# Performance work log

Measured on AMD Instinct MI355X. Metric: run time of the kernel, lower is better.

## Reference

```python
import jax, jax.numpy as jnp
import numpy as np
import math

H, W = 32, 32
HEAD = 8
ZONE = 2
D_MODEL = 512
BT, N, C = 8, H * W, D_MODEL
T = 4


def setup_inputs() -> dict:
    key = jax.random.key(0)
    ks = jax.random.split(key, 9)
    s = 1.0 / math.sqrt(D_MODEL)
    inp = {
        "x": jax.random.normal(ks[0], (BT, N, C), dtype=jnp.float32),
        "t": T,
        "Wq": jax.random.normal(ks[1], (C, C), dtype=jnp.float32) * s,
        "bq": jnp.zeros((C,), dtype=jnp.float32),
        "Wk": jax.random.normal(ks[2], (C, C), dtype=jnp.float32) * s,
        "bk": jnp.zeros((C,), dtype=jnp.float32),
        "Wv": jax.random.normal(ks[3], (C, C), dtype=jnp.float32) * s,
        "bv": jnp.zeros((C,), dtype=jnp.float32),
        "Wo": jax.random.normal(ks[4], (C, C), dtype=jnp.float32) * s,
        "bo": jnp.zeros((C,), dtype=jnp.float32),
    }
    return inp


def _to_windows(y, b, t, c_h):
    # [bt, n, c] -> [b, zone^2, head, t*(h/z)*(w/z), c_h]
    y = y.reshape(b, t, ZONE, H // ZONE, ZONE, W // ZONE, HEAD, c_h)
    y = jnp.transpose(y, (0, 2, 4, 6, 1, 3, 5, 7))
    return y.reshape(b, ZONE * ZONE, HEAD, -1, c_h)


def reference(x, t, Wq, bq, Wk, bk, Wv, bv, Wo, bo):
    bt, n, c = x.shape
    b = bt // t
    c_h = c // HEAD
    q = x @ Wq.T + bq
    k = x @ Wk.T + bk
    v = x @ Wv.T + bv
    q = _to_windows(q, b, t, c_h)  # [b, z^2, head, L, c_h]
    k = _to_windows(k, b, t, c_h)
    v = _to_windows(v, b, t, c_h)
    scores = jnp.einsum('bzhlc,bzhmc->bzhlm', q, k) / math.sqrt(c_h)
    p = jax.nn.softmax(scores, axis=-1)
    att = jnp.einsum('bzhlm,bzhmc->bzhlc', p, v)  # [b, z^2, head, L, c_h]
    att = att.reshape(b, ZONE, ZONE, HEAD, t, H // ZONE, W // ZONE, c_h)
    att = jnp.transpose(att, (0, 4, 1, 5, 2, 6, 3, 7)).reshape(bt, n, c)
    return att @ Wo.T + bo
```

## Files before the change

### kernel.cpp

```cpp
#include <hip/hip_runtime.h>
#include <math.h>
#include <stdint.h>


typedef unsigned short u16;
typedef unsigned int u32;
typedef __attribute__((ext_vector_type(8))) short bf16x8;
typedef __attribute__((ext_vector_type(4))) float f32x4;
typedef __attribute__((ext_vector_type(16))) float f32x16;

__device__ __forceinline__ u16 f2b(float f) {
  u32 u = __float_as_uint(f);
  return (u16)((u + 0x7FFFu + ((u >> 16) & 1u)) >> 16);
}

__device__ __forceinline__ void gld_lds16(const void* g, void* l) {
  auto gp = (__attribute__((address_space(1))) u32*)(uintptr_t)g;
  auto lp = (__attribute__((address_space(3))) u32*)(u32)(uintptr_t)l;
  __builtin_amdgcn_global_load_lds(gp, lp, 16, 0, 0);
}

__global__ __launch_bounds__(256)
void prep_cvt(const float* __restrict__ x, const float* __restrict__ wq,
              const float* __restrict__ wk, const float* __restrict__ wv,
              const float* __restrict__ wo, u16* __restrict__ xb,
              u16* __restrict__ wqb, u16* __restrict__ wkb,
              u16* __restrict__ wvb, u16* __restrict__ wob)
{
  int i = blockIdx.x * 256 + threadIdx.x;
  const float* src; u16* dst; int off;
  if (i < 1048576) { src = x; dst = xb; off = i; }
  else {
    int j = i - 1048576; int w = j >> 16; off = j & 65535;
    src = (w == 0) ? wq : (w == 1) ? wk : (w == 2) ? wv : wo;
    dst = (w == 0) ? wqb : (w == 1) ? wkb : (w == 2) ? wvb : wob;
  }
  float4 v = ((const float4*)src)[off];
  ushort4 o;
  o.x = f2b(v.x); o.y = f2b(v.y); o.z = f2b(v.z); o.w = f2b(v.w);
  ((ushort4*)dst)[off] = o;
}

__global__ __launch_bounds__(256, 2)
void gemm_qkv(const u16* __restrict__ A, const u16* __restrict__ Bq,
              const u16* __restrict__ Bk, const u16* __restrict__ Bv,
              const float* __restrict__ bq, const float* __restrict__ bk,
              const float* __restrict__ bv, u16* __restrict__ qw,
              u16* __restrict__ kw, u16* __restrict__ vt)
{
  __shared__ u16 As[2][8192];
  __shared__ u16 Ws[3][2][4096];
  const int tid = threadIdx.x;
  const int lane = tid & 63;
  const int wbase = (tid & 192) * 8;
  const int m0 = blockIdx.y * 128, n0 = blockIdx.x * 64;
  const int wm = ((tid >> 7) & 1) * 64;
  const int wn = ((tid >> 6) & 1) * 32;
  const int arow = tid >> 3, aslot = tid & 7;

  f32x4 accq[4][2], acck[4][2], accv[4][2];
#pragma unroll
  for (int i = 0; i < 4; ++i)
#pragma unroll
    for (int j = 0; j < 2; ++j) {
#pragma unroll
      for (int r = 0; r < 4; ++r) { accq[i][j][r] = 0.f; acck[i][j][r] = 0.f; accv[i][j][r] = 0.f; }
    }

  auto stage = [&](int t, int buf) {
#pragma unroll
    for (int q = 0; q < 4; ++q) {
      int row = q * 32 + arow;
      int sl = aslot ^ (row & 7);
      gld_lds16(A + (size_t)(m0 + row) * 512 + t * 64 + sl * 8,
                &As[buf][q * 2048 + wbase]);
    }
    const u16* bp[3] = {Bq, Bk, Bv};
#pragma unroll
    for (int w = 0; w < 3; ++w)
#pragma unroll
      for (int q = 0; q < 2; ++q) {
        int row = q * 32 + arow;
        int sl = aslot ^ (row & 7);
        gld_lds16(bp[w] + (size_t)(n0 + row) * 512 + t * 64 + sl * 8,
                  &Ws[w][buf][q * 2048 + wbase]);
      }
  };

  stage(0, 0);
  __syncthreads();
  int cur = 0;
#pragma unroll 1
  for (int t = 0; t < 8; ++t) {
    if (t < 7) stage(t + 1, cur ^ 1);
    const u16* la = As[cur];
    bf16x8 af[4][2];
#pragma unroll
    for (int mf = 0; mf < 4; ++mf)
#pragma unroll
      for (int ks = 0; ks < 2; ++ks) {
        int row = wm + mf * 16 + (lane & 15);
        int s = ks * 4 + (lane >> 4);
        af[mf][ks] = *(const bf16x8*)(la + row * 64 + ((s ^ (row & 7)) << 3));
      }
    __builtin_amdgcn_s_setprio(1);
#pragma unroll
    for (int ks = 0; ks < 2; ++ks)
#pragma unroll
      for (int nf = 0; nf < 2; ++nf) {
        int row = wn + nf * 16 + (lane & 15);
        int s = ks * 4 + (lane >> 4);
        int boff = row * 64 + ((s ^ (row & 7)) << 3);
        bf16x8 bq8 = *(const bf16x8*)(Ws[0][cur] + boff);
        bf16x8 bk8 = *(const bf16x8*)(Ws[1][cur] + boff);
        bf16x8 bv8 = *(const bf16x8*)(Ws[2][cur] + boff);
#pragma unroll
        for (int mf = 0; mf < 4; ++mf) {
          accq[mf][nf] = __builtin_amdgcn_mfma_f32_16x16x32_bf16(af[mf][ks], bq8, accq[mf][nf], 0, 0, 0);
          acck[mf][nf] = __builtin_amdgcn_mfma_f32_16x16x32_bf16(af[mf][ks], bk8, acck[mf][nf], 0, 0, 0);
          accv[mf][nf] = __builtin_amdgcn_mfma_f32_16x16x32_bf16(af[mf][ks], bv8, accv[mf][nf], 0, 0, 0);
        }
      }
    __builtin_amdgcn_s_setprio(0);
    __syncthreads();
    cur ^= 1;
  }

  int h[2], d[2]; float bqv[2], bkv[2], bvv[2];
#pragma unroll
  for (int nf = 0; nf < 2; ++nf) {
    int col = n0 + wn + nf * 16 + (lane & 15);
    h[nf] = col >> 6; d[nf] = col & 63;
    bqv[nf] = bq[col]; bkv[nf] = bk[col]; bvv[nf] = bv[col];
  }
#pragma unroll
  for (int mf = 0; mf < 4; ++mf) {
    int mb = m0 + wm + mf * 16 + ((lane >> 4) << 2);
    int b = mb >> 12, t = (mb >> 10) & 3, row32 = (mb >> 5) & 31, col32 = mb & 31;
    int zi = row32 >> 4, hirow = row32 & 15, zj = col32 >> 4, wj = col32 & 15;
    int gb = b * 32 + (zi * 2 + zj) * 8;
    int l0 = t * 256 + hirow * 16 + wj;
#pragma unroll
    for (int nf = 0; nf < 2; ++nf) {
      size_t qkbase = ((size_t)(gb + h[nf]) * 1024 + l0) * 64 + d[nf];
#pragma unroll
      for (int r = 0; r < 4; ++r) {
        qw[qkbase + (size_t)r * 64] = f2b(accq[mf][nf][r] + bqv[nf]);
        kw[qkbase + (size_t)r * 64] = f2b(acck[mf][nf][r] + bkv[nf]);
      }
      ushort4 pv;
      pv.x = f2b(accv[mf][nf][0] + bvv[nf]);
      pv.y = f2b(accv[mf][nf][1] + bvv[nf]);
      pv.z = f2b(accv[mf][nf][2] + bvv[nf]);
      pv.w = f2b(accv[mf][nf][3] + bvv[nf]);
      *(ushort4*)(vt + ((size_t)(gb + h[nf]) * 64 + d[nf]) * 1024 + l0) = pv;
    }
  }
}

__global__ __launch_bounds__(256)
void attn32(const u16* __restrict__ qw, const u16* __restrict__ kw,
            const u16* __restrict__ vt, u16* __restrict__ attb)
{
  __shared__ u16 Kl[3][4096];
  __shared__ u16 Vl[3][4096];

  const int tid = threadIdx.x, lane = tid & 63, wid = tid >> 6;
  const int hi = lane >> 5, ln = lane & 31;
  const int n = blockIdx.x;
  const int work = (n & 7) * 64 + (n >> 3);
  const int g = work >> 3, qt = work & 7;
  const int b = g >> 5, z = (g >> 3) & 3, h = g & 7, zi = z >> 1, zj = z & 1;
  const u16* qg = qw + (size_t)g * 65536;
  const u16* kg = kw + (size_t)g * 65536;
  const u16* vg = vt + (size_t)g * 65536;
  const int q0 = qt * 128 + wid * 32;
  const float SC2 = 0.125f * 1.44269504089f;
  const float SHIFT = -20.f;

  const int t8 = lane >> 3, s8 = lane & 7;

  auto stageKV = [&](int c, int buf) {
#pragma unroll
    for (int p = 0; p < 2; ++p) {
      int row = wid * 16 + p * 8 + t8;
      gld_lds16(kg + (size_t)(c * 64 + row) * 64 + ((s8 ^ (row & 7)) << 3),
                Kl[buf] + wid * 1024 + p * 512);
      gld_lds16(vg + (size_t)row * 1024 + c * 64 + ((s8 ^ (row & 7)) << 3),
                Vl[buf] + wid * 1024 + p * 512);
    }
  };

  bf16x8 qf[4];
#pragma unroll
  for (int ks = 0; ks < 4; ++ks)
    qf[ks] = *(const bf16x8*)(qg + (size_t)(q0 + ln) * 64 + ks * 16 + hi * 8);

  f32x16 o[2];
#pragma unroll
  for (int nf = 0; nf < 2; ++nf)
#pragma unroll
    for (int r = 0; r < 16; ++r) o[nf][r] = 0.f;
  float lrun = 0.f;

  stageKV(0, 0);
  stageKV(1, 1);
  asm volatile("s_waitcnt vmcnt(4)" ::: "memory");
  __builtin_amdgcn_s_barrier();
  __builtin_amdgcn_sched_barrier(0);

  int cur = 0, pre = 2;

#pragma unroll 1
  for (int c = 0; c < 16; ++c) {
    if (c < 14) stageKV(c + 2, pre);

    bf16x8 kk[2][4];
#pragma unroll
    for (int kb = 0; kb < 2; ++kb)
#pragma unroll
      for (int ks = 0; ks < 4; ++ks) {
        int row = kb * 32 + ln;
        int sl = (ks * 2 + hi) ^ (ln & 7);
        kk[kb][ks] = *(const bf16x8*)(Kl[cur] + row * 64 + sl * 8);
      }

    f32x16 st[2];
#pragma unroll
    for (int kb = 0; kb < 2; ++kb)
#pragma unroll
      for (int r = 0; r < 16; ++r) st[kb][r] = 0.f;
    __builtin_amdgcn_s_setprio(1);
#pragma unroll
    for (int ks = 0; ks < 4; ++ks) {
      st[0] = __builtin_amdgcn_mfma_f32_32x32x16_bf16(kk[0][ks], qf[ks], st[0], 0, 0, 0);
      st[1] = __builtin_amdgcn_mfma_f32_32x32x16_bf16(kk[1][ks], qf[ks], st[1], 0, 0, 0);
    }
    __builtin_amdgcn_s_setprio(0);

    float racc[4] = {0.f, 0.f, 0.f, 0.f};
#pragma unroll
    for (int kb = 0; kb < 2; ++kb)
#pragma unroll
      for (int r = 0; r < 16; ++r) {
        float p = exp2f(fmaf(st[kb][r], SC2, SHIFT));
        st[kb][r] = p;
        racc[r & 3] += p;
      }
    float rs = (racc[0] + racc[1]) + (racc[2] + racc[3]);
    rs += __shfl_xor(rs, 32);
    lrun += rs;

    u32 W[2][4][2];
#pragma unroll
    for (int kb = 0; kb < 2; ++kb)
#pragma unroll
      for (int j = 0; j < 4; ++j)
#pragma unroll
        for (int u = 0; u < 2; ++u) {
          u32 w;
          asm("v_cvt_pk_bf16_f32 %0, %1, %2"
              : "=v"(w) : "v"(st[kb][4 * j + 2 * u]), "v"(st[kb][4 * j + 2 * u + 1]));
          W[kb][j][u] = w;
        }
    __builtin_amdgcn_s_setprio(1);
#pragma unroll
    for (int ks = 0; ks < 4; ++ks) {
      const int kb = ks >> 1, sl2 = ks & 1;
      u32 a0 = W[kb][2 * sl2][0], b0 = W[kb][2 * sl2 + 1][0];
      u32 a1 = W[kb][2 * sl2][1], b1 = W[kb][2 * sl2 + 1][1];
      asm volatile("v_permlane32_swap_b32 %0, %1" : "+v"(a0), "+v"(b0));
      asm volatile("v_permlane32_swap_b32 %0, %1" : "+v"(a1), "+v"(b1));
      union { u32 u[4]; bf16x8 v; } pu;
      pu.u[0] = a0; pu.u[1] = a1; pu.u[2] = b0; pu.u[3] = b1;
#pragma unroll
      for (int nf = 0; nf < 2; ++nf) {
        int drow = nf * 32 + ln;
        int vsl = (ks * 2 + hi) ^ (ln & 7);
        bf16x8 vf = *(const bf16x8*)(Vl[cur] + drow * 64 + vsl * 8);
        o[nf] = __builtin_amdgcn_mfma_f32_32x32x16_bf16(pu.v, vf, o[nf], 0, 0, 0);
      }
    }
    __builtin_amdgcn_s_setprio(0);

    if (c < 15) {
      if (c < 14) { asm volatile("s_waitcnt vmcnt(4)" ::: "memory"); }
      else        { asm volatile("s_waitcnt vmcnt(0)" ::: "memory"); }
      __builtin_amdgcn_s_barrier();
      __builtin_amdgcn_sched_barrier(0);
    }
    cur = (cur == 2) ? 0 : cur + 1;
    pre = (pre == 2) ? 0 : pre + 1;
  }

  const int rowbase = b * 4096 + zi * 512 + zj * 16;
  const int colbase = h * 64;
#pragma unroll
  for (int r = 0; r < 16; ++r) {
    int qr = (r & 3) + 8 * (r >> 2) + 4 * hi;
    float lv = __shfl(lrun, qr);
    float iv = 1.f / lv;
    int l = q0 + qr;
    int row = rowbase + ((l >> 8) << 10) + (((l >> 4) & 15) << 5) + (l & 15);
    size_t off = (size_t)row * 512 + colbase + ln;
    attb[off] = f2b(o[0][r] * iv);
    attb[off + 32] = f2b(o[1][r] * iv);
  }
}

__global__ __launch_bounds__(256, 2)
void gemm_o(const u16* __restrict__ A, const u16* __restrict__ B,
            const float* __restrict__ bias, float* __restrict__ Cout)
{
  __shared__ u16 lds[2][12288];
  const int tid = threadIdx.x;
  const int lane = tid & 63;
  const int wbase = (tid & 192) * 8;
  const int m0 = blockIdx.y * 128, n0 = blockIdx.x * 64;
  const int wm = ((tid >> 7) & 1) * 64;
  const int wn = ((tid >> 6) & 1) * 32;
  const int arow = tid >> 3, aslot = tid & 7;

  f32x4 acc[4][2];
#pragma unroll
  for (int i = 0; i < 4; ++i)
#pragma unroll
    for (int j = 0; j < 2; ++j)
#pragma unroll
      for (int r = 0; r < 4; ++r) acc[i][j][r] = 0.f;

  auto stage = [&](int t, int buf) {
#pragma unroll
    for (int q = 0; q < 4; ++q) {
      int row = q * 32 + arow;
      int sl = aslot ^ (row & 7);
      gld_lds16(A + (size_t)(m0 + row) * 512 + t * 64 + sl * 8,
                &lds[buf][q * 2048 + wbase]);
    }
#pragma unroll
    for (int q = 0; q < 2; ++q) {
      int row = q * 32 + arow;
      int sl = aslot ^ (row & 7);
      gld_lds16(B + (size_t)(n0 + row) * 512 + t * 64 + sl * 8,
                &lds[buf][8192 + q * 2048 + wbase]);
    }
  };

  stage(0, 0);
  __syncthreads();
  int cur = 0;
#pragma unroll 1
  for (int t = 0; t < 8; ++t) {
    if (t < 7) stage(t + 1, cur ^ 1);
    const u16* la = lds[cur];
    const u16* lb = lds[cur] + 8192;
    bf16x8 af[4][2];
#pragma unroll
    for (int mf = 0; mf < 4; ++mf)
#pragma unroll
      for (int ks = 0; ks < 2; ++ks) {
        int row = wm + mf * 16 + (lane & 15);
        int s = ks * 4 + (lane >> 4);
        af[mf][ks] = *(const bf16x8*)(la + row * 64 + ((s ^ (row & 7)) << 3));
      }
    __builtin_amdgcn_s_setprio(1);
#pragma unroll
    for (int ks = 0; ks < 2; ++ks)
#pragma unroll
      for (int nf = 0; nf < 2; ++nf) {
        int row = wn + nf * 16 + (lane & 15);
        int s = ks * 4 + (lane >> 4);
        bf16x8 bfr = *(const bf16x8*)(lb + row * 64 + ((s ^ (row & 7)) << 3));
#pragma unroll
        for (int mf = 0; mf < 4; ++mf)
          acc[mf][nf] = __builtin_amdgcn_mfma_f32_16x16x32_bf16(af[mf][ks], bfr, acc[mf][nf], 0, 0, 0);
      }
    __builtin_amdgcn_s_setprio(0);
    __syncthreads();
    cur ^= 1;
  }

#pragma unroll
  for (int mf = 0; mf < 4; ++mf)
#pragma unroll
    for (int nf = 0; nf < 2; ++nf) {
      int row = m0 + wm + mf * 16 + ((lane >> 4) << 2);
      int col = n0 + wn + nf * 16 + (lane & 15);
      float bi = bias[col];
#pragma unroll
      for (int r = 0; r < 4; ++r)
        Cout[(size_t)(row + r) * 512 + col] = acc[mf][nf][r] + bi;
    }
}

extern "C" void kernel_launch(void* const* d_in, const int* in_sizes, int n_in,
                              void* d_out, int out_size, void* d_ws, size_t ws_size,
                              hipStream_t stream) {
  const float* x  = (const float*)d_in[0];
  const float* Wq = (const float*)d_in[2];
  const float* bq = (const float*)d_in[3];
  const float* Wk = (const float*)d_in[4];
  const float* bk = (const float*)d_in[5];
  const float* Wv = (const float*)d_in[6];
  const float* bv = (const float*)d_in[7];
  const float* Wo = (const float*)d_in[8];
  const float* bo = (const float*)d_in[9];

  u16* xb   = (u16*)d_ws;
  u16* wqb  = xb + 4194304;
  u16* wkb  = wqb + 262144;
  u16* wvb  = wkb + 262144;
  u16* wob  = wvb + 262144;
  u16* qwb  = wob + 262144;
  u16* kwb  = qwb + 4194304;
  u16* vtb  = kwb + 4194304;
  u16* attb = vtb + 4194304;

  prep_cvt<<<5120, 256, 0, stream>>>(x, Wq, Wk, Wv, Wo, xb, wqb, wkb, wvb, wob);
  gemm_qkv<<<dim3(8, 64), 256, 0, stream>>>(xb, wqb, wkb, wvb, bq, bk, bv, qwb, kwb, vtb);
  attn32<<<512, 256, 0, stream>>>(qwb, kwb, vtb, attb);
  gemm_o<<<dim3(8, 64), 256, 0, stream>>>(attb, wob, bo, (float*)d_out);
}
```

Before: 86.56 us.

## Process KV chunks in pairs with double-buffered LDS and two blocks per CU

Restructures the attention loop so each iteration handles two 64-key chunks. Both QK^T products are issued before the two softmax/PV stages, which gives more independent MFMA work to interleave. The LDS buffering changes from a 3-deep ring to a double buffer of chunk pairs, which halves the number of barriers per key. It also adds a launch bound of 2 blocks per CU, so register use is capped and the kernel may spill. The waits now drain all loads (vmcnt(0)) before each barrier, which could expose load latency.

```diff
diff --git a/kernel.cpp b/kernel.cpp
--- a/kernel.cpp
+++ b/kernel.cpp
@@ -158,12 +158,12 @@
   }
 }
 
-__global__ __launch_bounds__(256)
+__global__ __launch_bounds__(256, 2)
 void attn32(const u16* __restrict__ qw, const u16* __restrict__ kw,
             const u16* __restrict__ vt, u16* __restrict__ attb)
 {
-  __shared__ u16 Kl[3][4096];
-  __shared__ u16 Vl[3][4096];
+  __shared__ u16 Kl[2][2][4096];
+  __shared__ u16 Vl[2][2][4096];
 
   const int tid = threadIdx.x, lane = tid & 63, wid = tid >> 6;
   const int hi = lane >> 5, ln = lane & 31;
@@ -180,14 +180,14 @@
 
   const int t8 = lane >> 3, s8 = lane & 7;
 
-  auto stageKV = [&](int c, int buf) {
+  auto stageKV = [&](int c, int pb, int hf) {
 #pragma unroll
     for (int p = 0; p < 2; ++p) {
       int row = wid * 16 + p * 8 + t8;
       gld_lds16(kg + (size_t)(c * 64 + row) * 64 + ((s8 ^ (row & 7)) << 3),
-                Kl[buf] + wid * 1024 + p * 512);
+                Kl[pb][hf] + wid * 1024 + p * 512);
       gld_lds16(vg + (size_t)row * 1024 + c * 64 + ((s8 ^ (row & 7)) << 3),
-                Vl[buf] + wid * 1024 + p * 512);
+                Vl[pb][hf] + wid * 1024 + p * 512);
     }
   };
 
@@ -203,18 +203,7 @@
     for (int r = 0; r < 16; ++r) o[nf][r] = 0.f;
   float lrun = 0.f;
 
-  stageKV(0, 0);
-  stageKV(1, 1);
-  asm volatile("s_waitcnt vmcnt(4)" ::: "memory");
-  __builtin_amdgcn_s_barrier();
-  __builtin_amdgcn_sched_barrier(0);
-
-  int cur = 0, pre = 2;
-
-#pragma unroll 1
-  for (int c = 0; c < 16; ++c) {
-    if (c < 14) stageKV(c + 2, pre);
-
+  auto qkt = [&](const u16* Kb, f32x16 (&st)[2]) {
     bf16x8 kk[2][4];
 #pragma unroll
     for (int kb = 0; kb < 2; ++kb)
@@ -222,10 +211,8 @@
       for (int ks = 0; ks < 4; ++ks) {
         int row = kb * 32 + ln;
         int sl = (ks * 2 + hi) ^ (ln & 7);
-        kk[kb][ks] = *(const bf16x8*)(Kl[cur] + row * 64 + sl * 8);
-      }
-
-    f32x16 st[2];
+        kk[kb][ks] = *(const bf16x8*)(Kb + row * 64 + sl * 8);
+      }
 #pragma unroll
     for (int kb = 0; kb < 2; ++kb)
 #pragma unroll
@@ -237,7 +224,9 @@
       st[1] = __builtin_amdgcn_mfma_f32_32x32x16_bf16(kk[1][ks], qf[ks], st[1], 0, 0, 0);
     }
     __builtin_amdgcn_s_setprio(0);
-
+  };
+
+  auto softmax_pv = [&](f32x16 (&st)[2], const u16* Vb) -> float {
     float racc[4] = {0.f, 0.f, 0.f, 0.f};
 #pragma unroll
     for (int kb = 0; kb < 2; ++kb)
@@ -247,10 +236,6 @@
         st[kb][r] = p;
         racc[r & 3] += p;
       }
-    float rs = (racc[0] + racc[1]) + (racc[2] + racc[3]);
-    rs += __shfl_xor(rs, 32);
-    lrun += rs;
-
     u32 W[2][4][2];
 #pragma unroll
     for (int kb = 0; kb < 2; ++kb)
@@ -277,20 +262,39 @@
       for (int nf = 0; nf < 2; ++nf) {
         int drow = nf * 32 + ln;
         int vsl = (ks * 2 + hi) ^ (ln & 7);
-        bf16x8 vf = *(const bf16x8*)(Vl[cur] + drow * 64 + vsl * 8);
+        bf16x8 vf = *(const bf16x8*)(Vb + drow * 64 + vsl * 8);
         o[nf] = __builtin_amdgcn_mfma_f32_32x32x16_bf16(pu.v, vf, o[nf], 0, 0, 0);
       }
     }
     __builtin_amdgcn_s_setprio(0);
-
-    if (c < 15) {
-      if (c < 14) { asm volatile("s_waitcnt vmcnt(4)" ::: "memory"); }
-      else        { asm volatile("s_waitcnt vmcnt(0)" ::: "memory"); }
+    return (racc[0] + racc[1]) + (racc[2] + racc[3]);
+  };
+
+  stageKV(0, 0, 0);
+  stageKV(1, 0, 1);
+  asm volatile("s_waitcnt vmcnt(0)" ::: "memory");
+  __builtin_amdgcn_s_barrier();
+  __builtin_amdgcn_sched_barrier(0);
+
+#pragma unroll 1
+  for (int cp = 0; cp < 8; ++cp) {
+    const int pb = cp & 1;
+    if (cp < 7) { stageKV(2 * cp + 2, pb ^ 1, 0); stageKV(2 * cp + 3, pb ^ 1, 1); }
+
+    f32x16 stA[2], stB[2];
+    qkt(Kl[pb][0], stA);
+    qkt(Kl[pb][1], stB);
+    float rsA = softmax_pv(stA, Vl[pb][0]);
+    float rsB = softmax_pv(stB, Vl[pb][1]);
+    float rs = rsA + rsB;
+    rs += __shfl_xor(rs, 32);
+    lrun += rs;
+
+    if (cp < 7) {
+      asm volatile("s_waitcnt vmcnt(0)" ::: "memory");
       __builtin_amdgcn_s_barrier();
       __builtin_amdgcn_sched_barrier(0);
     }
-    cur = (cur == 2) ? 0 : cur + 1;
-    pre = (pre == 2) ? 0 : pre + 1;
   }
 
   const int rowbase = b * 4096 + zi * 512 + zj * 16;
```

After: 81.98 us. 5.3% less time.

## Process two query tiles per wave in attention to reuse K/V fragments

Applied to the files above, without the earlier changes.

Each wave in the attention kernel now handles 64 query rows as two 32-row tiles, so every K and V fragment read from LDS feeds twice as many MFMAs, and the grid is halved to 256 blocks. K/V staging drops from triple to double buffering with a full vmcnt(0) wait each iteration, and launch bounds request 2 blocks per CU. The aim is to cut LDS traffic and K/V global loads per query. In exchange it doubles accumulator register use, halves the number of blocks for 256 CUs, and exposes more load latency.

```diff
diff --git a/kernel.cpp b/kernel.cpp
--- a/kernel.cpp
+++ b/kernel.cpp
@@ -158,23 +158,23 @@
   }
 }
 
-__global__ __launch_bounds__(256)
+__global__ __launch_bounds__(256, 2)
 void attn32(const u16* __restrict__ qw, const u16* __restrict__ kw,
             const u16* __restrict__ vt, u16* __restrict__ attb)
 {
-  __shared__ u16 Kl[3][4096];
-  __shared__ u16 Vl[3][4096];
+  __shared__ u16 Kl[2][4096];
+  __shared__ u16 Vl[2][4096];
 
   const int tid = threadIdx.x, lane = tid & 63, wid = tid >> 6;
   const int hi = lane >> 5, ln = lane & 31;
   const int n = blockIdx.x;
-  const int work = (n & 7) * 64 + (n >> 3);
-  const int g = work >> 3, qt = work & 7;
+  const int work = (n & 7) * 32 + (n >> 3);
+  const int g = work >> 2, qt = work & 3;
   const int b = g >> 5, z = (g >> 3) & 3, h = g & 7, zi = z >> 1, zj = z & 1;
   const u16* qg = qw + (size_t)g * 65536;
   const u16* kg = kw + (size_t)g * 65536;
   const u16* vg = vt + (size_t)g * 65536;
-  const int q0 = qt * 128 + wid * 32;
+  const int q0 = qt * 256 + wid * 64;
   const float SC2 = 0.125f * 1.44269504089f;
   const float SHIFT = -20.f;
 
@@ -191,53 +191,23 @@
     }
   };
 
-  bf16x8 qf[4];
-#pragma unroll
-  for (int ks = 0; ks < 4; ++ks)
-    qf[ks] = *(const bf16x8*)(qg + (size_t)(q0 + ln) * 64 + ks * 16 + hi * 8);
-
-  f32x16 o[2];
-#pragma unroll
-  for (int nf = 0; nf < 2; ++nf)
-#pragma unroll
-    for (int r = 0; r < 16; ++r) o[nf][r] = 0.f;
-  float lrun = 0.f;
-
-  stageKV(0, 0);
-  stageKV(1, 1);
-  asm volatile("s_waitcnt vmcnt(4)" ::: "memory");
-  __builtin_amdgcn_s_barrier();
-  __builtin_amdgcn_sched_barrier(0);
-
-  int cur = 0, pre = 2;
-
-#pragma unroll 1
-  for (int c = 0; c < 16; ++c) {
-    if (c < 14) stageKV(c + 2, pre);
-
-    bf16x8 kk[2][4];
-#pragma unroll
-    for (int kb = 0; kb < 2; ++kb)
-#pragma unroll
-      for (int ks = 0; ks < 4; ++ks) {
-        int row = kb * 32 + ln;
-        int sl = (ks * 2 + hi) ^ (ln & 7);
-        kk[kb][ks] = *(const bf16x8*)(Kl[cur] + row * 64 + sl * 8);
-      }
-
-    f32x16 st[2];
-#pragma unroll
-    for (int kb = 0; kb < 2; ++kb)
-#pragma unroll
-      for (int r = 0; r < 16; ++r) st[kb][r] = 0.f;
-    __builtin_amdgcn_s_setprio(1);
-#pragma unroll
-    for (int ks = 0; ks < 4; ++ks) {
-      st[0] = __builtin_amdgcn_mfma_f32_32x32x16_bf16(kk[0][ks], qf[ks], st[0], 0, 0, 0);
-      st[1] = __builtin_amdgcn_mfma_f32_32x32x16_bf16(kk[1][ks], qf[ks], st[1], 0, 0, 0);
-    }
-    __builtin_amdgcn_s_setprio(0);
-
+  bf16x8 qf[2][4];
+#pragma unroll
+  for (int t = 0; t < 2; ++t)
+#pragma unroll
+    for (int ks = 0; ks < 4; ++ks)
+      qf[t][ks] = *(const bf16x8*)(qg + (size_t)(q0 + t * 32 + ln) * 64 + ks * 16 + hi * 8);
+
+  f32x16 o[2][2];
+#pragma unroll
+  for (int t = 0; t < 2; ++t)
+#pragma unroll
+    for (int nf = 0; nf < 2; ++nf)
+#pragma unroll
+      for (int r = 0; r < 16; ++r) o[t][nf][r] = 0.f;
+  float lrun[2] = {0.f, 0.f};
+
+  auto softmax_pack = [&](f32x16 (&st)[2], bf16x8 (&pa)[4]) -> float {
     float racc[4] = {0.f, 0.f, 0.f, 0.f};
 #pragma unroll
     for (int kb = 0; kb < 2; ++kb)
@@ -247,10 +217,6 @@
         st[kb][r] = p;
         racc[r & 3] += p;
       }
-    float rs = (racc[0] + racc[1]) + (racc[2] + racc[3]);
-    rs += __shfl_xor(rs, 32);
-    lrun += rs;
-
     u32 W[2][4][2];
 #pragma unroll
     for (int kb = 0; kb < 2; ++kb)
@@ -263,7 +229,6 @@
               : "=v"(w) : "v"(st[kb][4 * j + 2 * u]), "v"(st[kb][4 * j + 2 * u + 1]));
           W[kb][j][u] = w;
         }
-    __builtin_amdgcn_s_setprio(1);
 #pragma unroll
     for (int ks = 0; ks < 4; ++ks) {
       const int kb = ks >> 1, sl2 = ks & 1;
@@ -273,38 +238,102 @@
       asm volatile("v_permlane32_swap_b32 %0, %1" : "+v"(a1), "+v"(b1));
       union { u32 u[4]; bf16x8 v; } pu;
       pu.u[0] = a0; pu.u[1] = a1; pu.u[2] = b0; pu.u[3] = b1;
+      pa[ks] = pu.v;
+    }
+    return (racc[0] + racc[1]) + (racc[2] + racc[3]);
+  };
+
+  stageKV(0, 0);
+  asm volatile("s_waitcnt vmcnt(0)" ::: "memory");
+  __builtin_amdgcn_s_barrier();
+  __builtin_amdgcn_sched_barrier(0);
+  int cur = 0;
+
+#pragma unroll 1
+  for (int c = 0; c < 16; ++c) {
+    if (c < 15) stageKV(c + 1, cur ^ 1);
+
+    bf16x8 kk[2][4];
+#pragma unroll
+    for (int kb = 0; kb < 2; ++kb)
+#pragma unroll
+      for (int ks = 0; ks < 4; ++ks) {
+        int row = kb * 32 + ln;
+        int sl = (ks * 2 + hi) ^ (ln & 7);
+        kk[kb][ks] = *(const bf16x8*)(Kl[cur] + row * 64 + sl * 8);
+      }
+
+    f32x16 st[2][2];
+#pragma unroll
+    for (int t = 0; t < 2; ++t)
+#pragma unroll
+      for (int kb = 0; kb < 2; ++kb)
+#pragma unroll
+        for (int r = 0; r < 16; ++r) st[t][kb][r] = 0.f;
+    __builtin_amdgcn_s_setprio(1);
+#pragma unroll
+    for (int ks = 0; ks < 4; ++ks) {
+      st[0][0] = __builtin_amdgcn_mfma_f32_32x32x16_bf16(kk[0][ks], qf[0][ks], st[0][0], 0, 0, 0);
+      st[0][1] = __builtin_amdgcn_mfma_f32_32x32x16_bf16(kk[1][ks], qf[0][ks], st[0][1], 0, 0, 0);
+      st[1][0] = __builtin_amdgcn_mfma_f32_32x32x16_bf16(kk[0][ks], qf[1][ks], st[1][0], 0, 0, 0);
+      st[1][1] = __builtin_amdgcn_mfma_f32_32x32x16_bf16(kk[1][ks], qf[1][ks], st[1][1], 0, 0, 0);
+    }
+    __builtin_amdgcn_s_setprio(0);
+
+    bf16x8 vf[4][2];
+#pragma unroll
+    for (int ks = 0; ks < 4; ++ks)
 #pragma unroll
       for (int nf = 0; nf < 2; ++nf) {
         int drow = nf * 32 + ln;
         int vsl = (ks * 2 + hi) ^ (ln & 7);
-        bf16x8 vf = *(const bf16x8*)(Vl[cur] + drow * 64 + vsl * 8);
-        o[nf] = __builtin_amdgcn_mfma_f32_32x32x16_bf16(pu.v, vf, o[nf], 0, 0, 0);
-      }
+        vf[ks][nf] = *(const bf16x8*)(Vl[cur] + drow * 64 + vsl * 8);
+      }
+
+    bf16x8 paA[4];
+    lrun[0] += softmax_pack(st[0], paA);
+    __builtin_amdgcn_s_setprio(1);
+#pragma unroll
+    for (int ks = 0; ks < 4; ++ks) {
+      o[0][0] = __builtin_amdgcn_mfma_f32_32x32x16_bf16(paA[ks], vf[ks][0], o[0][0], 0, 0, 0);
+      o[0][1] = __builtin_amdgcn_mfma_f32_32x32x16_bf16(paA[ks], vf[ks][1], o[0][1], 0, 0, 0);
     }
     __builtin_amdgcn_s_setprio(0);
 
+    bf16x8 paB[4];
+    lrun[1] += softmax_pack(st[1], paB);
+    __builtin_amdgcn_s_setprio(1);
+#pragma unroll
+    for (int ks = 0; ks < 4; ++ks) {
+      o[1][0] = __builtin_amdgcn_mfma_f32_32x32x16_bf16(paB[ks], vf[ks][0], o[1][0], 0, 0, 0);
+      o[1][1] = __builtin_amdgcn_mfma_f32_32x32x16_bf16(paB[ks], vf[ks][1], o[1][1], 0, 0, 0);
+    }
+    __builtin_amdgcn_s_setprio(0);
+
     if (c < 15) {
-      if (c < 14) { asm volatile("s_waitcnt vmcnt(4)" ::: "memory"); }
-      else        { asm volatile("s_waitcnt vmcnt(0)" ::: "memory"); }
+      asm volatile("s_waitcnt vmcnt(0)" ::: "memory");
       __builtin_amdgcn_s_barrier();
       __builtin_amdgcn_sched_barrier(0);
     }
-    cur = (cur == 2) ? 0 : cur + 1;
-    pre = (pre == 2) ? 0 : pre + 1;
+    cur ^= 1;
   }
 
   const int rowbase = b * 4096 + zi * 512 + zj * 16;
   const int colbase = h * 64;
 #pragma unroll
-  for (int r = 0; r < 16; ++r) {
-    int qr = (r & 3) + 8 * (r >> 2) + 4 * hi;
-    float lv = __shfl(lrun, qr);
-    float iv = 1.f / lv;
-    int l = q0 + qr;
-    int row = rowbase + ((l >> 8) << 10) + (((l >> 4) & 15) << 5) + (l & 15);
-    size_t off = (size_t)row * 512 + colbase + ln;
-    attb[off] = f2b(o[0][r] * iv);
-    attb[off + 32] = f2b(o[1][r] * iv);
+  for (int t = 0; t < 2; ++t) {
+    float rt = lrun[t] + __shfl_xor(lrun[t], 32);
+#pragma unroll
+    for (int r = 0; r < 16; ++r) {
+      int qr = (r & 3) + 8 * (r >> 2) + 4 * hi;
+      float lv = __shfl(rt, qr);
+      float iv = 1.f / lv;
+      int l = q0 + t * 32 + qr;
+      int row = rowbase + ((l >> 8) << 10) + (((l >> 4) & 15) << 5) + (l & 15);
+      size_t off = (size_t)row * 512 + colbase + ln;
+      attb[off] = f2b(o[t][0][r] * iv);
+      attb[off + 32] = f2b(o[t][1][r] * iv);
+    }
   }
 }
 
@@ -418,6 +447,6 @@
 
   prep_cvt<<<5120, 256, 0, stream>>>(x, Wq, Wk, Wv, Wo, xb, wqb, wkb, wvb, wob);
   gemm_qkv<<<dim3(8, 64), 256, 0, stream>>>(xb, wqb, wkb, wvb, bq, bk, bv, qwb, kwb, vtb);
-  attn32<<<512, 256, 0, stream>>>(qwb, kwb, vtb, attb);
+  attn32<<<256, 256, 0, stream>>>(qwb, kwb, vtb, attb);
   gemm_o<<<dim3(8, 64), 256, 0, stream>>>(attb, wob, bo, (float*)d_out);
 }
```

After: 95.99 us. +10.9%, slower.
